# Kernel tuning notes

Hardware: AMD Instinct MI355X
Metric: run time of the kernel (lower is better)

Reference implementation:

```python
import jax, jax.numpy as jnp
import numpy as np

N_NODES = 100000


def _gcn_conv(x, W, b, src, dst, norm, n_nodes):
    # PyG GCNConv: linear transform, then normalized gather-scatter aggregation.
    h = x @ W                                   # [N, out]
    msg = h[src] * norm[:, None]                # gather along edges [E+N, out]
    agg = jax.ops.segment_sum(msg, dst, num_segments=n_nodes)
    return agg + b


def setup_inputs() -> dict:
    key = jax.random.key(0)
    ks = jax.random.split(key, 8)
    input_dim, hidden_dim, output_dim = 128, 64, 16
    n_edges = 1600000
    x = jax.random.normal(ks[0], (N_NODES, input_dim), dtype=jnp.float32)
    edge_index = jax.random.randint(ks[1], (2, n_edges), 0, N_NODES, dtype=jnp.int64)
    W1 = jax.random.normal(ks[2], (input_dim, hidden_dim), dtype=jnp.float32) / np.sqrt(input_dim)
    b1 = jnp.zeros((hidden_dim,), dtype=jnp.float32)
    W2 = jax.random.normal(ks[3], (hidden_dim, hidden_dim), dtype=jnp.float32) / np.sqrt(hidden_dim)
    b2 = jnp.zeros((hidden_dim,), dtype=jnp.float32)
    Wc = jax.random.normal(ks[4], (hidden_dim, output_dim), dtype=jnp.float32) / np.sqrt(hidden_dim)
    bc = jnp.zeros((output_dim,), dtype=jnp.float32)
    return {"x": x, "edge_index": edge_index, "W1": W1, "b1": b1,
            "W2": W2, "b2": b2, "Wc": Wc, "bc": bc}


def reference(x, edge_index, W1, b1, W2, b2, Wc, bc):
    n = x.shape[0]
    # gcn_norm: add self-loops, symmetric D^{-1/2} (A+I) D^{-1/2} normalization
    loops = jnp.arange(n, dtype=edge_index.dtype)
    src = jnp.concatenate([edge_index[0], loops])
    dst = jnp.concatenate([edge_index[1], loops])
    deg = jax.ops.segment_sum(jnp.ones_like(dst, dtype=x.dtype), dst, num_segments=n)
    deg_isqrt = jnp.where(deg > 0, jax.lax.rsqrt(deg), 0.0)
    norm = deg_isqrt[src] * deg_isqrt[dst]      # [E+N]

    h = _gcn_conv(x, W1, b1, src, dst, norm, n)
    h = jax.nn.relu(h)
    # dropout p=0.3 is identity in eval mode (reference baseline is deterministic)
    h = _gcn_conv(h, W2, b2, src, dst, norm, n)
    out = h @ Wc + bc
    return out
```

## Files before the change

kernel.cpp:

```cpp
#include <hip/hip_runtime.h>


constexpr int ID = 128;
constexpr int HD = 64;
constexpr int OD = 16;
constexpr int RB = 512;
constexpr int KMAX = 256;
constexpr int CHUNK = 4096;

typedef _Float16 f16x8 __attribute__((ext_vector_type(8)));
typedef _Float16 f16x4 __attribute__((ext_vector_type(4)));
typedef float    f32x4 __attribute__((ext_vector_type(4)));

__global__ __launch_bounds__(256) void passA_kernel(const int4* __restrict__ dst4,
                                                    int* __restrict__ cnt, int E4, int K) {
    __shared__ int h[KMAX];
    int tid = threadIdx.x;
    for (int i = tid; i < K; i += 256) h[i] = 0;
    __syncthreads();
    int id = blockIdx.x * 256 + tid, n = gridDim.x * 256;
    for (int i = id; i < E4; i += n) {
        int4 d = dst4[i];
        atomicAdd(&h[d.x >> 9], 1); atomicAdd(&h[d.y >> 9], 1);
        atomicAdd(&h[d.z >> 9], 1); atomicAdd(&h[d.w >> 9], 1);
    }
    __syncthreads();
    for (int i = tid; i < K; i += 256) if (h[i]) atomicAdd(&cnt[i], h[i]);
}

__global__ __launch_bounds__(256) void cscan_kernel(const int* __restrict__ cnt,
                                                    int* __restrict__ coff,
                                                    int* __restrict__ cursor, int K, int E) {
    __shared__ int ts[KMAX];
    int tid = threadIdx.x;
    int v = (tid < K) ? cnt[tid] : 0;
    ts[tid] = v; __syncthreads();
    for (int d = 1; d < KMAX; d <<= 1) {
        int t = (tid >= d) ? ts[tid - d] : 0;
        __syncthreads();
        ts[tid] += t;
        __syncthreads();
    }
    if (tid < K) { int excl = ts[tid] - v; coff[tid] = excl; cursor[tid] = excl; }
    if (tid == 0) coff[K] = E;
}

__global__ __launch_bounds__(256) void passB_kernel(const int* __restrict__ src,
                                                    const int* __restrict__ dst,
                                                    int* __restrict__ cursor,
                                                    unsigned* __restrict__ epk, int E) {
    __shared__ unsigned      buf[CHUNK];
    __shared__ unsigned char bkt[CHUNK];
    __shared__ int hist[KMAX], lofs[KMAX], gpos[KMAX], ts[KMAX];
    int tid = threadIdx.x;
    int base = blockIdx.x * CHUNK;
    int cnt = min(CHUNK, E - base);

    for (int i = tid; i < KMAX; i += 256) hist[i] = 0;
    __syncthreads();

    unsigned mypay[CHUNK / 256];
    short    myb[CHUNK / 256];
    short    myrank[CHUNK / 256];
    #pragma unroll
    for (int j = 0; j < CHUNK / 256; ++j) {
        int o = j * 256 + tid;
        myb[j] = -1;
        if (o < cnt) {
            int d = dst[base + o], s = src[base + o];
            int b = d >> 9;
            myb[j] = (short)b;
            myrank[j] = (short)atomicAdd(&hist[b], 1);
            mypay[j] = ((unsigned)(d & (RB - 1)) << 17) | (unsigned)s;
        }
    }
    __syncthreads();

    int v = hist[tid];
    ts[tid] = v; __syncthreads();
    for (int d = 1; d < KMAX; d <<= 1) {
        int t = (tid >= d) ? ts[tid - d] : 0;
        __syncthreads();
        ts[tid] += t;
        __syncthreads();
    }
    lofs[tid] = ts[tid] - v;
    if (v > 0) gpos[tid] = atomicAdd(&cursor[tid], v);
    __syncthreads();

    #pragma unroll
    for (int j = 0; j < CHUNK / 256; ++j) {
        if (myb[j] >= 0) {
            int pos = lofs[myb[j]] + myrank[j];
            buf[pos] = mypay[j];
            bkt[pos] = (unsigned char)myb[j];
        }
    }
    __syncthreads();

    for (int i = tid; i < cnt; i += 256) {
        int b = bkt[i];
        epk[gpos[b] + (i - lofs[b])] = buf[i];
    }
}

__global__ __launch_bounds__(512) void sortB_kernel(
    const int* __restrict__ coff, const unsigned* __restrict__ epk,
    int* __restrict__ sse, int* __restrict__ off,
    float* __restrict__ dinv, int N) {
    __shared__ int hist[RB];
    __shared__ int lofs[RB];
    __shared__ int ts[RB];
    int b = blockIdx.x, tid = threadIdx.x, base = b * RB;
    hist[tid] = 0;
    __syncthreads();
    int e0 = coff[b], e1 = coff[b + 1];
    for (int e = e0 + tid; e < e1; e += 512)
        atomicAdd(&hist[epk[e] >> 17], 1);
    __syncthreads();
    int v = hist[tid];
    ts[tid] = v; __syncthreads();
    for (int d = 1; d < RB; d <<= 1) {
        int t = (tid >= d) ? ts[tid - d] : 0;
        __syncthreads();
        ts[tid] += t;
        __syncthreads();
    }
    {
        int excl = ts[tid] - v;
        int node = base + tid;
        if (node <= N) off[node] = e0 + excl;
        if (node < N)  dinv[node] = rsqrtf((float)v + 1.0f);
        lofs[tid] = e0 + excl;
    }
    __syncthreads();
    for (int e = e0 + tid; e < e1; e += 512) {
        unsigned pk = epk[e];
        int pos = atomicAdd(&lofs[pk >> 17], 1);
        sse[pos] = (int)(pk & 0x1FFFF);
    }
}

__global__ __launch_bounds__(256) void prep_kernel(const float* __restrict__ W1,
                                                   const float* __restrict__ W2,
                                                   _Float16* __restrict__ w1t,
                                                   _Float16* __restrict__ w2t) {
    int id = blockIdx.x * 256 + threadIdx.x, n = gridDim.x * 256;
    for (int i = id; i < ID * HD; i += n) {
        int k = i >> 6, c = i & 63;
        w1t[c * ID + k] = (_Float16)W1[i];
    }
    for (int i = id; i < HD * HD; i += n) {
        int k = i >> 6, c = i & 63;
        w2t[c * HD + k] = (_Float16)W2[i];
    }
}

__global__ __launch_bounds__(256) void gemm1_kernel(
    const float* __restrict__ x, const _Float16* __restrict__ w1t,
    const float* __restrict__ dinv, _Float16* __restrict__ th, int N) {
    __shared__ __align__(16) _Float16 xh[64 * ID];
    __shared__ __align__(16) _Float16 wh[HD * ID];
    int tid = threadIdx.x;
    int base = blockIdx.x * 64;
    #pragma unroll
    for (int it = 0; it < 4; ++it) {
        int idx = (it * 256 + tid) * 8;
        int r = idx >> 7, c = idx & 127;
        f16x8 v = *(const f16x8*)&w1t[idx];
        *(f16x8*)&wh[r * ID + (c ^ ((r & 7) << 3))] = v;
    }
    #pragma unroll
    for (int it = 0; it < 4; ++it) {
        int idx = (it * 256 + tid) * 8;
        int r = idx >> 7, c = idx & 127;
        int row = base + r;
        f16x8 h;
        if (row < N) {
            float4 a = *(const float4*)&x[(size_t)row * ID + c];
            float4 b = *(const float4*)&x[(size_t)row * ID + c + 4];
            h[0] = (_Float16)a.x; h[1] = (_Float16)a.y;
            h[2] = (_Float16)a.z; h[3] = (_Float16)a.w;
            h[4] = (_Float16)b.x; h[5] = (_Float16)b.y;
            h[6] = (_Float16)b.z; h[7] = (_Float16)b.w;
        } else {
            #pragma unroll
            for (int j = 0; j < 8; ++j) h[j] = (_Float16)0.f;
        }
        *(f16x8*)&xh[r * ID + (c ^ ((r & 7) << 3))] = h;
    }
    __syncthreads();
    int lane = tid & 63, wv = tid >> 6;
    int lr = lane & 15, g = lane >> 4;
    f32x4 z = {0.f, 0.f, 0.f, 0.f};
    f32x4 acc[4] = {z, z, z, z};
    #pragma unroll
    for (int kk = 0; kk < 4; ++kk) {
        int kb = kk * 32 + g * 8;
        int ar = wv * 16 + lr;
        f16x8 af = *(const f16x8*)&xh[ar * ID + (kb ^ ((ar & 7) << 3))];
        #pragma unroll
        for (int ct = 0; ct < 4; ++ct) {
            int br = ct * 16 + lr;
            f16x8 bf = *(const f16x8*)&wh[br * ID + (kb ^ ((br & 7) << 3))];
            acc[ct] = __builtin_amdgcn_mfma_f32_16x16x32_f16(af, bf, acc[ct], 0, 0, 0);
        }
    }
    int r0 = base + wv * 16 + g * 4;
    #pragma unroll
    for (int j = 0; j < 4; ++j) {
        int row = r0 + j;
        if (row < N) {
            float dd = dinv[row];
            #pragma unroll
            for (int ct = 0; ct < 4; ++ct)
                th[(size_t)row * HD + ct * 16 + lr] = (_Float16)(acc[ct][j] * dd);
        }
    }
}

__global__ __launch_bounds__(256) void pull_kernel(
    const int* __restrict__ off, const int* __restrict__ sse,
    const float* __restrict__ dinv, const _Float16* __restrict__ th,
    float* __restrict__ a, int N) {
    int lane = threadIdx.x & 63;
    int w = (blockIdx.x * blockDim.x + threadIdx.x) >> 6;
    if (w >= N) return;
    int sub = lane >> 4;
    int fl  = lane & 15;
    const f16x4* th4 = (const f16x4*)th;
    int o0 = off[w], o1 = off[w + 1];
    float ax = 0.f, ay = 0.f, az = 0.f, aw = 0.f;
    int j = o0;
    while (j < o1) {
        int nb = min(64, o1 - j);
        int sidx = (lane < nb) ? sse[j + lane] : 0;
        int i = 0;
        for (; i + 15 < nb; i += 16) {
            int s0 = __shfl(sidx, i + sub);
            int s1 = __shfl(sidx, i + 4 + sub);
            int s2 = __shfl(sidx, i + 8 + sub);
            int s3 = __shfl(sidx, i + 12 + sub);
            f16x4 v0 = th4[(size_t)s0 * 16 + fl];
            f16x4 v1 = th4[(size_t)s1 * 16 + fl];
            f16x4 v2 = th4[(size_t)s2 * 16 + fl];
            f16x4 v3 = th4[(size_t)s3 * 16 + fl];
            ax += ((float)v0[0] + (float)v1[0]) + ((float)v2[0] + (float)v3[0]);
            ay += ((float)v0[1] + (float)v1[1]) + ((float)v2[1] + (float)v3[1]);
            az += ((float)v0[2] + (float)v1[2]) + ((float)v2[2] + (float)v3[2]);
            aw += ((float)v0[3] + (float)v1[3]) + ((float)v2[3] + (float)v3[3]);
        }
        for (; i < nb; i += 4) {
            int e = i + sub;
            int s = __shfl(sidx, (e < nb) ? e : (nb - 1));
            if (e < nb) {
                f16x4 v = th4[(size_t)s * 16 + fl];
                ax += (float)v[0]; ay += (float)v[1];
                az += (float)v[2]; aw += (float)v[3];
            }
        }
        j += nb;
    }
    ax += __shfl_xor(ax, 16); ax += __shfl_xor(ax, 32);
    ay += __shfl_xor(ay, 16); ay += __shfl_xor(ay, 32);
    az += __shfl_xor(az, 16); az += __shfl_xor(az, 32);
    aw += __shfl_xor(aw, 16); aw += __shfl_xor(aw, 32);
    if (sub == 0) {
        f16x4 sv = th4[(size_t)w * 16 + fl];
        float dd = dinv[w];
        float4 o;
        o.x = dd * (ax + (float)sv[0]);
        o.y = dd * (ay + (float)sv[1]);
        o.z = dd * (az + (float)sv[2]);
        o.w = dd * (aw + (float)sv[3]);
        *(float4*)&a[(size_t)w * HD + fl * 4] = o;
    }
}

__global__ __launch_bounds__(256) void gemm2_kernel(
    const float* __restrict__ ain, const _Float16* __restrict__ w2t,
    const float* __restrict__ bias, const float* __restrict__ dinv,
    _Float16* __restrict__ th, int N) {
    __shared__ __align__(16) _Float16 ah[64 * HD];
    __shared__ __align__(16) _Float16 wh[HD * HD];
    int tid = threadIdx.x;
    int base = blockIdx.x * 64;
    #pragma unroll
    for (int it = 0; it < 2; ++it) {
        int idx = (it * 256 + tid) * 8;
        int r = idx >> 6, c = idx & 63;
        f16x8 v = *(const f16x8*)&w2t[idx];
        *(f16x8*)&wh[r * HD + (c ^ ((r & 7) << 3))] = v;
    }
    #pragma unroll
    for (int it = 0; it < 2; ++it) {
        int idx = (it * 256 + tid) * 8;
        int r = idx >> 6, c = idx & 63;
        int row = base + r;
        f16x8 h;
        if (row < N) {
            float4 a = *(const float4*)&ain[(size_t)row * HD + c];
            float4 b = *(const float4*)&ain[(size_t)row * HD + c + 4];
            h[0] = (_Float16)fmaxf(a.x + bias[c + 0], 0.f);
            h[1] = (_Float16)fmaxf(a.y + bias[c + 1], 0.f);
            h[2] = (_Float16)fmaxf(a.z + bias[c + 2], 0.f);
            h[3] = (_Float16)fmaxf(a.w + bias[c + 3], 0.f);
            h[4] = (_Float16)fmaxf(b.x + bias[c + 4], 0.f);
            h[5] = (_Float16)fmaxf(b.y + bias[c + 5], 0.f);
            h[6] = (_Float16)fmaxf(b.z + bias[c + 6], 0.f);
            h[7] = (_Float16)fmaxf(b.w + bias[c + 7], 0.f);
        } else {
            #pragma unroll
            for (int j = 0; j < 8; ++j) h[j] = (_Float16)0.f;
        }
        *(f16x8*)&ah[r * HD + (c ^ ((r & 7) << 3))] = h;
    }
    __syncthreads();
    int lane = tid & 63, wv = tid >> 6;
    int lr = lane & 15, g = lane >> 4;
    f32x4 z = {0.f, 0.f, 0.f, 0.f};
    f32x4 acc[4] = {z, z, z, z};
    #pragma unroll
    for (int kk = 0; kk < 2; ++kk) {
        int kb = kk * 32 + g * 8;
        int ar = wv * 16 + lr;
        f16x8 af = *(const f16x8*)&ah[ar * HD + (kb ^ ((ar & 7) << 3))];
        #pragma unroll
        for (int ct = 0; ct < 4; ++ct) {
            int br = ct * 16 + lr;
            f16x8 bf = *(const f16x8*)&wh[br * HD + (kb ^ ((br & 7) << 3))];
            acc[ct] = __builtin_amdgcn_mfma_f32_16x16x32_f16(af, bf, acc[ct], 0, 0, 0);
        }
    }
    int r0 = base + wv * 16 + g * 4;
    #pragma unroll
    for (int j = 0; j < 4; ++j) {
        int row = r0 + j;
        if (row < N) {
            float dd = dinv[row];
            #pragma unroll
            for (int ct = 0; ct < 4; ++ct)
                th[(size_t)row * HD + ct * 16 + lr] = (_Float16)(acc[ct][j] * dd);
        }
    }
}

__global__ __launch_bounds__(256) void final_kernel(
    const float* __restrict__ ain, const float* __restrict__ b2,
    const float* __restrict__ Wc, const float* __restrict__ bc,
    float* __restrict__ out, int N) {
    __shared__ float Ws[HD * OD];
    __shared__ float hs[16][HD + 1];
    int tid = threadIdx.x;
    for (int i = tid; i < HD * OD; i += 256) Ws[i] = Wc[i];
    int base = blockIdx.x * 16;
    for (int i = tid; i < 16 * HD; i += 256) {
        int r = i >> 6, c = i & 63;
        int row = base + r;
        hs[r][c] = (row < N) ? ain[(size_t)row * HD + c] + b2[c] : 0.0f;
    }
    __syncthreads();
    int col = tid & 15, r = tid >> 4;
    int row = base + r;
    if (row < N) {
        float acc = bc[col];
        #pragma unroll
        for (int k = 0; k < HD; ++k)
            acc += hs[r][k] * Ws[k * OD + col];
        out[(size_t)row * OD + col] = acc;
    }
}

extern "C" void kernel_launch(void* const* d_in, const int* in_sizes, int n_in,
                              void* d_out, int out_size, void* d_ws, size_t ws_size,
                              hipStream_t stream) {
    const float* x  = (const float*)d_in[0];
    const int*   ei = (const int*)d_in[1];
    const float* W1 = (const float*)d_in[2];
    const float* b1 = (const float*)d_in[3];
    const float* W2 = (const float*)d_in[4];
    const float* b2 = (const float*)d_in[5];
    const float* Wc = (const float*)d_in[6];
    const float* bc = (const float*)d_in[7];
    float* out = (float*)d_out;

    int N = in_sizes[0] / ID;
    int E = in_sizes[1] / 2;
    const int* src = ei;
    const int* dst = ei + E;
    int K = (N + RB - 1) / RB;
    int Npad = (N + 63) & ~63;

    char* p = (char*)d_ws;
    int*      cnt    = (int*)p;      p += KMAX * 4;
    int*      coff   = (int*)p;      p += (KMAX + 4) * 4;
    int*      cursor = (int*)p;      p += KMAX * 4;
    float*    dinv   = (float*)p;    p += (size_t)Npad * 4;
    int*      off    = (int*)p;      p += (size_t)(Npad + RB) * 4;
    _Float16* w1t    = (_Float16*)p; p += (size_t)HD * ID * 2;
    _Float16* w2t    = (_Float16*)p; p += (size_t)HD * HD * 2;
    unsigned* epk    = (unsigned*)p; p += (size_t)E * 4;
    int*      sse    = (int*)p;      p += (size_t)E * 4;
    _Float16* th     = (_Float16*)p; p += (size_t)N * HD * 2;
    float*    a1     = (float*)p;    p += (size_t)N * HD * 4;

    hipMemsetAsync(cnt, 0, (size_t)K * sizeof(int), stream);

    passA_kernel<<<512, 256, 0, stream>>>((const int4*)dst, cnt, E / 4, K);
    prep_kernel<<<32, 256, 0, stream>>>(W1, W2, w1t, w2t);
    cscan_kernel<<<1, KMAX, 0, stream>>>(cnt, coff, cursor, K, E);
    passB_kernel<<<(E + CHUNK - 1) / CHUNK, 256, 0, stream>>>(src, dst, cursor, epk, E);
    sortB_kernel<<<K, RB, 0, stream>>>(coff, epk, sse, off, dinv, N);

    gemm1_kernel<<<(N + 63) / 64, 256, 0, stream>>>(x, w1t, dinv, th, N);
    pull_kernel<<<(N * 64 + 255) / 256, 256, 0, stream>>>(off, sse, dinv, th, a1, N);

    gemm2_kernel<<<(N + 63) / 64, 256, 0, stream>>>(a1, w2t, b1, dinv, th, N);
    pull_kernel<<<(N * 64 + 255) / 256, 256, 0, stream>>>(off, sse, dinv, th, a1, N);

    final_kernel<<<(N + 15) / 16, 256, 0, stream>>>(a1, b2, Wc, bc, out, N);
}
```

Before: 294.4 us.

## Split aggregation into two feature-half passes, store aggregates in fp16, merge prep and scan

The gather-aggregation is split into two launches, each covering half of the 64 features, with 8 edges in flight per wave instead of 4. The intent is to halve the gathered working set per pass so the random row reads fit better in cache. The aggregate buffer becomes fp16, which halves its write and read traffic in gemm2 and final, at some cost in precision. The weight prep and the count scan are merged into one launch, and the split costs an extra pass over offsets and indices.

Result: slower. 358.6 us (+21.8%).

```diff
diff --git a/kernel.cpp b/kernel.cpp
--- a/kernel.cpp
+++ b/kernel.cpp
@@ -28,21 +28,35 @@
     for (int i = tid; i < K; i += 256) if (h[i]) atomicAdd(&cnt[i], h[i]);
 }
 
-__global__ __launch_bounds__(256) void cscan_kernel(const int* __restrict__ cnt,
-                                                    int* __restrict__ coff,
-                                                    int* __restrict__ cursor, int K, int E) {
-    __shared__ int ts[KMAX];
-    int tid = threadIdx.x;
-    int v = (tid < K) ? cnt[tid] : 0;
-    ts[tid] = v; __syncthreads();
-    for (int d = 1; d < KMAX; d <<= 1) {
-        int t = (tid >= d) ? ts[tid - d] : 0;
-        __syncthreads();
-        ts[tid] += t;
-        __syncthreads();
-    }
-    if (tid < K) { int excl = ts[tid] - v; coff[tid] = excl; cursor[tid] = excl; }
-    if (tid == 0) coff[K] = E;
+__global__ __launch_bounds__(256) void prepscan_kernel(
+    const float* __restrict__ W1, const float* __restrict__ W2,
+    _Float16* __restrict__ w1t, _Float16* __restrict__ w2t,
+    const int* __restrict__ cnt, int* __restrict__ coff,
+    int* __restrict__ cursor, int K, int E) {
+    int tid = threadIdx.x;
+    if (blockIdx.x < 32) {
+        int id = blockIdx.x * 256 + tid, n = 32 * 256;
+        for (int i = id; i < ID * HD; i += n) {
+            int k = i >> 6, c = i & 63;
+            w1t[c * ID + k] = (_Float16)W1[i];
+        }
+        for (int i = id; i < HD * HD; i += n) {
+            int k = i >> 6, c = i & 63;
+            w2t[c * HD + k] = (_Float16)W2[i];
+        }
+    } else {
+        __shared__ int ts[KMAX];
+        int v = (tid < K) ? cnt[tid] : 0;
+        ts[tid] = v; __syncthreads();
+        for (int d = 1; d < KMAX; d <<= 1) {
+            int t = (tid >= d) ? ts[tid - d] : 0;
+            __syncthreads();
+            ts[tid] += t;
+            __syncthreads();
+        }
+        if (tid < K) { int excl = ts[tid] - v; coff[tid] = excl; cursor[tid] = excl; }
+        if (tid == 0) coff[K] = E;
+    }
 }
 
 __global__ __launch_bounds__(256) void passB_kernel(const int* __restrict__ src,
@@ -138,21 +152,6 @@
         unsigned pk = epk[e];
         int pos = atomicAdd(&lofs[pk >> 17], 1);
         sse[pos] = (int)(pk & 0x1FFFF);
-    }
-}
-
-__global__ __launch_bounds__(256) void prep_kernel(const float* __restrict__ W1,
-                                                   const float* __restrict__ W2,
-                                                   _Float16* __restrict__ w1t,
-                                                   _Float16* __restrict__ w2t) {
-    int id = blockIdx.x * 256 + threadIdx.x, n = gridDim.x * 256;
-    for (int i = id; i < ID * HD; i += n) {
-        int k = i >> 6, c = i & 63;
-        w1t[c * ID + k] = (_Float16)W1[i];
-    }
-    for (int i = id; i < HD * HD; i += n) {
-        int k = i >> 6, c = i & 63;
-        w2t[c * HD + k] = (_Float16)W2[i];
     }
 }
 
@@ -219,16 +218,17 @@
     }
 }
 
-__global__ __launch_bounds__(256) void pull_kernel(
+__global__ __launch_bounds__(256) void pull_half_kernel(
     const int* __restrict__ off, const int* __restrict__ sse,
     const float* __restrict__ dinv, const _Float16* __restrict__ th,
-    float* __restrict__ a, int N) {
+    _Float16* __restrict__ a, int N, int half) {
     int lane = threadIdx.x & 63;
     int w = (blockIdx.x * blockDim.x + threadIdx.x) >> 6;
     if (w >= N) return;
-    int sub = lane >> 4;
-    int fl  = lane & 15;
+    int sub = lane >> 3;
+    int fl  = lane & 7;
     const f16x4* th4 = (const f16x4*)th;
+    size_t hoff = (size_t)(half << 3) + fl;
     int o0 = off[w], o1 = off[w + 1];
     float ax = 0.f, ay = 0.f, az = 0.f, aw = 0.f;
     int j = o0;
@@ -236,49 +236,59 @@
         int nb = min(64, o1 - j);
         int sidx = (lane < nb) ? sse[j + lane] : 0;
         int i = 0;
-        for (; i + 15 < nb; i += 16) {
+        for (; i + 31 < nb; i += 32) {
             int s0 = __shfl(sidx, i + sub);
-            int s1 = __shfl(sidx, i + 4 + sub);
-            int s2 = __shfl(sidx, i + 8 + sub);
-            int s3 = __shfl(sidx, i + 12 + sub);
-            f16x4 v0 = th4[(size_t)s0 * 16 + fl];
-            f16x4 v1 = th4[(size_t)s1 * 16 + fl];
-            f16x4 v2 = th4[(size_t)s2 * 16 + fl];
-            f16x4 v3 = th4[(size_t)s3 * 16 + fl];
+            int s1 = __shfl(sidx, i + 8 + sub);
+            int s2 = __shfl(sidx, i + 16 + sub);
+            int s3 = __shfl(sidx, i + 24 + sub);
+            f16x4 v0 = th4[(size_t)s0 * 16 + hoff];
+            f16x4 v1 = th4[(size_t)s1 * 16 + hoff];
+            f16x4 v2 = th4[(size_t)s2 * 16 + hoff];
+            f16x4 v3 = th4[(size_t)s3 * 16 + hoff];
             ax += ((float)v0[0] + (float)v1[0]) + ((float)v2[0] + (float)v3[0]);
             ay += ((float)v0[1] + (float)v1[1]) + ((float)v2[1] + (float)v3[1]);
             az += ((float)v0[2] + (float)v1[2]) + ((float)v2[2] + (float)v3[2]);
             aw += ((float)v0[3] + (float)v1[3]) + ((float)v2[3] + (float)v3[3]);
         }
-        for (; i < nb; i += 4) {
+        for (; i + 15 < nb; i += 16) {
+            int s0 = __shfl(sidx, i + sub);
+            int s1 = __shfl(sidx, i + 8 + sub);
+            f16x4 v0 = th4[(size_t)s0 * 16 + hoff];
+            f16x4 v1 = th4[(size_t)s1 * 16 + hoff];
+            ax += (float)v0[0] + (float)v1[0];
+            ay += (float)v0[1] + (float)v1[1];
+            az += (float)v0[2] + (float)v1[2];
+            aw += (float)v0[3] + (float)v1[3];
+        }
+        for (; i < nb; i += 8) {
             int e = i + sub;
             int s = __shfl(sidx, (e < nb) ? e : (nb - 1));
             if (e < nb) {
-                f16x4 v = th4[(size_t)s * 16 + fl];
+                f16x4 v = th4[(size_t)s * 16 + hoff];
                 ax += (float)v[0]; ay += (float)v[1];
                 az += (float)v[2]; aw += (float)v[3];
             }
         }
         j += nb;
     }
-    ax += __shfl_xor(ax, 16); ax += __shfl_xor(ax, 32);
-    ay += __shfl_xor(ay, 16); ay += __shfl_xor(ay, 32);
-    az += __shfl_xor(az, 16); az += __shfl_xor(az, 32);
-    aw += __shfl_xor(aw, 16); aw += __shfl_xor(aw, 32);
+    ax += __shfl_xor(ax, 8); ax += __shfl_xor(ax, 16); ax += __shfl_xor(ax, 32);
+    ay += __shfl_xor(ay, 8); ay += __shfl_xor(ay, 16); ay += __shfl_xor(ay, 32);
+    az += __shfl_xor(az, 8); az += __shfl_xor(az, 16); az += __shfl_xor(az, 32);
+    aw += __shfl_xor(aw, 8); aw += __shfl_xor(aw, 16); aw += __shfl_xor(aw, 32);
     if (sub == 0) {
-        f16x4 sv = th4[(size_t)w * 16 + fl];
+        f16x4 sv = th4[(size_t)w * 16 + hoff];
         float dd = dinv[w];
-        float4 o;
-        o.x = dd * (ax + (float)sv[0]);
-        o.y = dd * (ay + (float)sv[1]);
-        o.z = dd * (az + (float)sv[2]);
-        o.w = dd * (aw + (float)sv[3]);
-        *(float4*)&a[(size_t)w * HD + fl * 4] = o;
+        f16x4 o;
+        o[0] = (_Float16)(dd * (ax + (float)sv[0]));
+        o[1] = (_Float16)(dd * (ay + (float)sv[1]));
+        o[2] = (_Float16)(dd * (az + (float)sv[2]));
+        o[3] = (_Float16)(dd * (aw + (float)sv[3]));
+        ((f16x4*)a)[(size_t)w * 16 + hoff] = o;
     }
 }
 
 __global__ __launch_bounds__(256) void gemm2_kernel(
-    const float* __restrict__ ain, const _Float16* __restrict__ w2t,
+    const _Float16* __restrict__ ain, const _Float16* __restrict__ w2t,
     const float* __restrict__ bias, const float* __restrict__ dinv,
     _Float16* __restrict__ th, int N) {
     __shared__ __align__(16) _Float16 ah[64 * HD];
@@ -299,19 +309,13 @@
         int row = base + r;
         f16x8 h;
         if (row < N) {
-            float4 a = *(const float4*)&ain[(size_t)row * HD + c];
-            float4 b = *(const float4*)&ain[(size_t)row * HD + c + 4];
-            h[0] = (_Float16)fmaxf(a.x + bias[c + 0], 0.f);
-            h[1] = (_Float16)fmaxf(a.y + bias[c + 1], 0.f);
-            h[2] = (_Float16)fmaxf(a.z + bias[c + 2], 0.f);
-            h[3] = (_Float16)fmaxf(a.w + bias[c + 3], 0.f);
-            h[4] = (_Float16)fmaxf(b.x + bias[c + 4], 0.f);
-            h[5] = (_Float16)fmaxf(b.y + bias[c + 5], 0.f);
-            h[6] = (_Float16)fmaxf(b.z + bias[c + 6], 0.f);
-            h[7] = (_Float16)fmaxf(b.w + bias[c + 7], 0.f);
+            f16x8 v = *(const f16x8*)&ain[(size_t)row * HD + c];
+            #pragma unroll
+            for (int jj = 0; jj < 8; ++jj)
+                h[jj] = (_Float16)fmaxf((float)v[jj] + bias[c + jj], 0.f);
         } else {
             #pragma unroll
-            for (int j = 0; j < 8; ++j) h[j] = (_Float16)0.f;
+            for (int jj = 0; jj < 8; ++jj) h[jj] = (_Float16)0.f;
         }
         *(f16x8*)&ah[r * HD + (c ^ ((r & 7) << 3))] = h;
     }
@@ -346,7 +350,7 @@
 }
 
 __global__ __launch_bounds__(256) void final_kernel(
-    const float* __restrict__ ain, const float* __restrict__ b2,
+    const _Float16* __restrict__ ain, const float* __restrict__ b2,
     const float* __restrict__ Wc, const float* __restrict__ bc,
     float* __restrict__ out, int N) {
     __shared__ float Ws[HD * OD];
@@ -354,10 +358,18 @@
     int tid = threadIdx.x;
     for (int i = tid; i < HD * OD; i += 256) Ws[i] = Wc[i];
     int base = blockIdx.x * 16;
-    for (int i = tid; i < 16 * HD; i += 256) {
-        int r = i >> 6, c = i & 63;
+    for (int i = tid; i < 128; i += 256) {
+        int r = i >> 3, c = (i & 7) * 8;
         int row = base + r;
-        hs[r][c] = (row < N) ? ain[(size_t)row * HD + c] + b2[c] : 0.0f;
+        if (row < N) {
+            f16x8 v = *(const f16x8*)&ain[(size_t)row * HD + c];
+            #pragma unroll
+            for (int jj = 0; jj < 8; ++jj)
+                hs[r][c + jj] = (float)v[jj] + b2[c + jj];
+        } else {
+            #pragma unroll
+            for (int jj = 0; jj < 8; ++jj) hs[r][c + jj] = 0.f;
+        }
     }
     __syncthreads();
     int col = tid & 15, r = tid >> 4;
@@ -402,21 +414,24 @@
     unsigned* epk    = (unsigned*)p; p += (size_t)E * 4;
     int*      sse    = (int*)p;      p += (size_t)E * 4;
     _Float16* th     = (_Float16*)p; p += (size_t)N * HD * 2;
-    float*    a1     = (float*)p;    p += (size_t)N * HD * 4;
+    _Float16* a1     = (_Float16*)p; p += (size_t)N * HD * 2;
 
     hipMemsetAsync(cnt, 0, (size_t)K * sizeof(int), stream);
 
     passA_kernel<<<512, 256, 0, stream>>>((const int4*)dst, cnt, E / 4, K);
-    prep_kernel<<<32, 256, 0, stream>>>(W1, W2, w1t, w2t);
-    cscan_kernel<<<1, KMAX, 0, stream>>>(cnt, coff, cursor, K, E);
+    prepscan_kernel<<<33, 256, 0, stream>>>(W1, W2, w1t, w2t, cnt, coff, cursor, K, E);
     passB_kernel<<<(E + CHUNK - 1) / CHUNK, 256, 0, stream>>>(src, dst, cursor, epk, E);
     sortB_kernel<<<K, RB, 0, stream>>>(coff, epk, sse, off, dinv, N);
 
+    int pgrid = (N * 64 + 255) / 256;
+
     gemm1_kernel<<<(N + 63) / 64, 256, 0, stream>>>(x, w1t, dinv, th, N);
-    pull_kernel<<<(N * 64 + 255) / 256, 256, 0, stream>>>(off, sse, dinv, th, a1, N);
+    pull_half_kernel<<<pgrid, 256, 0, stream>>>(off, sse, dinv, th, a1, N, 0);
+    pull_half_kernel<<<pgrid, 256, 0, stream>>>(off, sse, dinv, th, a1, N, 1);
 
     gemm2_kernel<<<(N + 63) / 64, 256, 0, stream>>>(a1, w2t, b1, dinv, th, N);
-    pull_kernel<<<(N * 64 + 255) / 256, 256, 0, stream>>>(off, sse, dinv, th, a1, N);
+    pull_half_kernel<<<pgrid, 256, 0, stream>>>(off, sse, dinv, th, a1, N, 0);
+    pull_half_kernel<<<pgrid, 256, 0, stream>>>(off, sse, dinv, th, a1, N, 1);
 
     final_kernel<<<(N + 15) / 16, 256, 0, stream>>>(a1, b2, Wc, bc, out, N);
 }
```
